# Kernel tuning notes

Measured on AMD Instinct MI355X. Metric: run time of the kernel, lower is better.

## Reference

```python
import jax, jax.numpy as jnp
import numpy as np

EPS_BN = 1e-5
EPS_COS = 1e-8
M_BINS = 10


def _bn(x, g, b):
    # eval-mode BatchNorm2d with running_mean=0, running_var=1
    s = g / jnp.sqrt(1.0 + EPS_BN)
    return x * s[None, :, None, None] + b[None, :, None, None]


def _dw(x, w, pad, dil):
    # depthwise conv, x [B,C,H,W], w [C,1,kh,kw]
    return jax.lax.conv_general_dilated(
        x, w, window_strides=(1, 1), padding=pad, rhs_dilation=dil,
        dimension_numbers=('NCHW', 'OIHW', 'NCHW'),
        feature_group_count=x.shape[1])


def setup_inputs() -> dict:
    key = jax.random.key(0)
    ks = jax.random.split(key, 20)
    B, INP, OUP, H, W = 16, 64, 64, 128, 128
    f32 = jnp.float32
    d = {}
    d['x'] = jax.random.normal(ks[0], (B, INP, H, W), f32)
    d['w_conv1'] = jax.random.normal(ks[1], (OUP, INP), f32) * 0.05
    d['pr_w1'] = jax.random.normal(ks[2], (OUP, 1, 1, 5), f32) * 0.2
    d['pr_w2'] = jax.random.normal(ks[3], (OUP, 1, 5, 1), f32) * 0.2
    d['pr_w3'] = jax.random.normal(ks[4], (OUP, 1, 1, 5), f32) * 0.2
    d['pr_w4'] = jax.random.normal(ks[5], (OUP, 1, 5, 1), f32) * 0.2
    d['pr_gamma'] = 1.0 + 0.1 * jax.random.normal(ks[6], (5, OUP), f32)
    d['pr_beta'] = 0.1 * jax.random.normal(ks[7], (5, OUP), f32)
    d['bn1_g'] = 1.0 + 0.1 * jax.random.normal(ks[8], (OUP,), f32)
    d['bn1_b'] = 0.1 * jax.random.normal(ks[9], (OUP,), f32)
    d['bn2_g'] = 1.0 + 0.1 * jax.random.normal(ks[10], (OUP,), f32)
    d['bn2_b'] = 0.1 * jax.random.normal(ks[11], (OUP,), f32)
    d['fc1_w'] = jax.random.normal(ks[12], (OUP, 2), f32) * 0.5
    d['fc1_b'] = 0.1 * jax.random.normal(ks[13], (OUP,), f32)
    d['phi1_w'] = jax.random.normal(ks[14], (OUP, OUP), f32) * 0.1
    d['phi1_b'] = 0.01 * jax.random.normal(ks[15], (OUP,), f32)
    d['phi2_w'] = jax.random.normal(ks[16], (OUP, OUP), f32) * 0.1
    d['phi2_b'] = 0.01 * jax.random.normal(ks[17], (OUP,), f32)
    d['phi3_w'] = jax.random.normal(ks[18], (OUP, OUP), f32) * 0.1
    d['phi3_b'] = 0.01 * jax.random.normal(ks[19], (OUP,), f32)
    d['w_conv2'] = jax.random.normal(jax.random.fold_in(key, 99), (OUP, 1), f32) * 0.1
    return d


def reference(x, w_conv1, pr_w1, pr_w2, pr_w3, pr_w4, pr_gamma, pr_beta,
              bn1_g, bn1_b, bn2_g, bn2_b, fc1_w, fc1_b,
              phi1_w, phi1_b, phi2_w, phi2_b, phi3_w, phi3_b, w_conv2):
    B, C, H, W = x.shape
    M = M_BINS
    OUP = w_conv1.shape[0]
    # conv1 (1x1) + Position_reinforcement branch
    x_c = jnp.einsum('oc,bchw->bohw', w_conv1, x)
    h = _bn(x_c, pr_gamma[0], pr_beta[0])
    h = _dw(h, pr_w1, ((0, 0), (2, 2)), (1, 1))
    h = _bn(h, pr_gamma[1], pr_beta[1])
    h = _dw(h, pr_w2, ((2, 2), (0, 0)), (1, 1))
    h = _bn(h, pr_gamma[2], pr_beta[2])
    h = _dw(h, pr_w3, ((0, 0), (4, 4)), (2, 2))
    h = _bn(h, pr_gamma[3], pr_beta[3])
    h = _dw(h, pr_w4, ((4, 4), (0, 0)), (2, 2))
    x_center = _bn(h, pr_gamma[4], pr_beta[4])
    # cosine similarity of each pixel feature with the global-avg feature
    g = jnp.mean(x, axis=(2, 3), keepdims=True)             # [B,C,1,1]
    num = jnp.sum(g * x, axis=1)                            # [B,H,W]
    gn = jnp.maximum(jnp.sqrt(jnp.sum(g * g, axis=1)), EPS_COS)
    xn = jnp.maximum(jnp.sqrt(jnp.sum(x * x, axis=1)), EPS_COS)
    S = num / (gn * xn)                                     # [B,H,W]
    Sf = S.reshape(B, H * W)
    # torch casts min/max with float() -> detached constants
    mn = jax.lax.stop_gradient(jnp.min(Sf, axis=1))
    mx = jax.lax.stop_gradient(jnp.max(Sf, axis=1))
    t = jnp.arange(M, dtype=x.dtype) / (M - 1)
    levels = mn[:, None] + (mx - mn)[:, None] * t[None, :]  # [B,M]
    diff = jnp.abs(levels[:, None, :] - Sf[:, :, None])     # [B,HW,M] soft bins
    V = jnp.where(diff < 0.5 / M, 1.0 - diff, jnp.zeros((), x.dtype))
    colsum = jnp.sum(V, axis=1)                             # [B,M]
    # torch normalizes by V.sum() while only columns 0..j are filled -> cumsum
    denom = jnp.cumsum(colsum, axis=1)
    Ch = jnp.stack([colsum / denom, levels], axis=-1)       # [B,M,2]
    Cf = Ch.reshape(-1, 2) @ fc1_w.T + fc1_b                # [B*M,OUP]
    Cq = Cf.reshape(B, OUP, M)                              # raw view as in torch
    p1 = jnp.einsum('oc,bcm->bom', phi1_w, Cq) + phi1_b[None, :, None]
    p2 = jnp.einsum('oc,bcm->bom', phi2_w, Cq) + phi2_b[None, :, None]
    X = jax.nn.softmax(jnp.einsum('bcm,bcn->bmn', p1, p2), axis=-1)  # [B,M,M]
    p3 = jnp.einsum('oc,bcm->bom', phi3_w, Cq) + phi3_b[None, :, None]
    Lp = jnp.einsum('bcm,bmn->bcn', p3, X)                  # [B,OUP,M]
    Vr = V.reshape(B, M, H * W)                             # raw view as in torch
    R = jnp.einsum('bcm,bmk->bck', Lp, Vr).reshape(B, OUP, H, W)
    x_tex = _bn(R, bn1_g, bn1_b)
    x_full = _bn(w_conv2[:, 0][None, :, None, None] * S[:, None, :, :], bn2_g, bn2_b)
    att = jax.nn.sigmoid(x_full + x_tex + x_center)
    return x * att
```

## Files before the change

### kernel.cpp

```cpp
#include <hip/hip_runtime.h>
#include <hip/hip_bf16.h>
#include <math.h>

#define NB   16
#define NC   64
#define NH   128
#define NW   128
#define NHW  16384
#define NM   10

__global__ __launch_bounds__(256) void k_gmean(const float* __restrict__ x,
                                               double* __restrict__ g) {
    int bc = blockIdx.x;
    const float* xp = x + (size_t)bc * NHW;
    double s = 0.0;
    for (int i = threadIdx.x; i < NHW / 4; i += 256) {
        float4 v = ((const float4*)xp)[i];
        s += (double)v.x + (double)v.y + (double)v.z + (double)v.w;
    }
    for (int off = 32; off; off >>= 1) s += __shfl_down(s, off);
    __shared__ double red[4];
    int wid = threadIdx.x >> 6, lane = threadIdx.x & 63;
    if (lane == 0) red[wid] = s;
    __syncthreads();
    if (threadIdx.x == 0)
        g[bc] = (red[0] + red[1] + red[2] + red[3]) * (1.0 / (double)NHW);
}

__global__ __launch_bounds__(256) void k_misc(const float* __restrict__ W,
                                              const double* __restrict__ g,
                                              float* __restrict__ Wt,
                                              double* __restrict__ gn) {
    if (blockIdx.x == 0) {
        for (int e = threadIdx.x; e < 64 * 64; e += 256) {
            int c = e >> 6, o = e & 63;
            Wt[c * 64 + o] = W[o * 64 + c];
        }
    } else if (threadIdx.x == 0) {
        int b = blockIdx.x - 1;
        const double* gb = g + b * NC;
        double gsq = 0.0;
        for (int c = 0; c < NC; ++c) gsq += gb[c] * gb[c];
        gn[b] = fmax(sqrt(gsq), 1e-8);
    }
}

__global__ __launch_bounds__(256) void k_conv1_S(
        const float* __restrict__ x, const float* __restrict__ Wt,
        const double* __restrict__ g, const double* __restrict__ gn,
        float* __restrict__ xc, double* __restrict__ S) {
    __shared__ __align__(16) float Xs[64 * 128];
    int bid = blockIdx.x;
    int b = bid >> 7, k0 = (bid & 127) * 128;
    int tid = threadIdx.x;
    const float* xb = x + (size_t)b * NC * NHW + k0;

    for (int e = tid; e < 64 * 32; e += 256) {
        int c = e >> 5, p4 = (e & 31) << 2;
        *(float4*)&Xs[c * 128 + p4] =
            *(const float4*)&xb[(size_t)c * NHW + p4];
    }
    __syncthreads();

    if (tid < 128) {
        const double* gb = g + b * NC;
        double num = 0.0, sq = 0.0;
#pragma unroll
        for (int c = 0; c < NC; ++c) {
            double v = (double)Xs[c * 128 + tid];
            num += gb[c] * v;
            sq  += v * v;
        }
        double xn = fmax(sqrt(sq), 1e-8);
        S[(size_t)b * NHW + k0 + tid] = num / (gn[b] * xn);
    }

    int o0 = __builtin_amdgcn_readfirstlane((tid >> 6) * 8);
    int px0 = (tid & 63) * 2;
    float acc[16][2];
#pragma unroll
    for (int i = 0; i < 16; ++i) { acc[i][0] = 0.f; acc[i][1] = 0.f; }

#pragma unroll 4
    for (int c = 0; c < NC; ++c) {
        float2 xa = *(float2*)&Xs[c * 128 + px0];
        const float* wr = Wt + c * 64 + o0;
        float wv[16];
#pragma unroll
        for (int i = 0; i < 8; ++i) wv[i] = wr[i];
#pragma unroll
        for (int i = 0; i < 8; ++i) wv[8 + i] = wr[32 + i];
#pragma unroll
        for (int i = 0; i < 16; ++i) {
            acc[i][0] = fmaf(wv[i], xa.x, acc[i][0]);
            acc[i][1] = fmaf(wv[i], xa.y, acc[i][1]);
        }
    }

    float* xcb = xc + (size_t)b * NC * NHW + k0;
#pragma unroll
    for (int i = 0; i < 16; ++i) {
        int o = o0 + ((i < 8) ? i : (24 + i));
        float2 s0; s0.x = acc[i][0]; s0.y = acc[i][1];
        *(float2*)&xcb[(size_t)o * NHW + px0] = s0;
    }
}

__global__ __launch_bounds__(256) void k_chain(
        const double* __restrict__ S,
        const float* __restrict__ fc1w, const float* __restrict__ fc1b,
        const float* __restrict__ ph1w, const float* __restrict__ ph1b,
        const float* __restrict__ ph2w, const float* __restrict__ ph2b,
        const float* __restrict__ ph3w, const float* __restrict__ ph3b,
        double* __restrict__ levelsOut, float* __restrict__ LpOut) {
    int b = blockIdx.x, tid = threadIdx.x;
    const double* Sb = S + b * NHW;

    double mn = 1e300, mx = -1e300;
    for (int i = tid; i < NHW; i += 256) {
        double v = Sb[i];
        mn = fmin(mn, v); mx = fmax(mx, v);
    }
    for (int off = 32; off; off >>= 1) {
        mn = fmin(mn, __shfl_down(mn, off));
        mx = fmax(mx, __shfl_down(mx, off));
    }
    __shared__ double rmn[4], rmx[4];
    int wid = tid >> 6, lane = tid & 63;
    if (lane == 0) { rmn[wid] = mn; rmx[wid] = mx; }
    __syncthreads();
    __shared__ double levS[NM];
    if (tid == 0) {
        double a = fmin(fmin(rmn[0], rmn[1]), fmin(rmn[2], rmn[3]));
        double z = fmax(fmax(rmx[0], rmx[1]), fmax(rmx[2], rmx[3]));
        for (int m = 0; m < NM; ++m) levS[m] = a + (z - a) * ((double)m / 9.0);
    }
    __syncthreads();
    double lv[NM];
#pragma unroll
    for (int m = 0; m < NM; ++m) lv[m] = levS[m];

    double bins[NM];
#pragma unroll
    for (int m = 0; m < NM; ++m) bins[m] = 0.0;
    for (int i = tid; i < NHW; i += 256) {
        double v = Sb[i];
#pragma unroll
        for (int m = 0; m < NM; ++m) {
            double d = fabs(lv[m] - v);
            if (d < 0.05) bins[m] += 1.0 - d;
        }
    }
#pragma unroll
    for (int m = 0; m < NM; ++m)
        for (int off = 32; off; off >>= 1) bins[m] += __shfl_down(bins[m], off);
    __shared__ double wb[4][NM];
    if (lane == 0) {
#pragma unroll
        for (int m = 0; m < NM; ++m) wb[wid][m] = bins[m];
    }
    __syncthreads();
    __shared__ float ratio[NM];
    if (tid == 0) {
        double den = 0.0;
        for (int m = 0; m < NM; ++m) {
            double cs = wb[0][m] + wb[1][m] + wb[2][m] + wb[3][m];
            den += cs;
            ratio[m] = (float)(cs / den);
        }
    }
    __syncthreads();

    __shared__ float CfL[640];
    for (int idx = tid; idx < 640; idx += 256) {
        int rm = idx >> 6, o = idx & 63;
        CfL[idx] = ratio[rm] * fc1w[o*2+0] + (float)levS[rm] * fc1w[o*2+1] + fc1b[o];
    }
    __syncthreads();

    __shared__ float P1[640], P2[640], P3[640];
    for (int idx = tid; idx < 640; idx += 256) {
        int o = idx / 10, m = idx - o * 10;
        float a1 = ph1b[o], a2 = ph2b[o], a3 = ph3b[o];
        for (int c2 = 0; c2 < NC; ++c2) {
            float cq = CfL[c2*10 + m];
            a1 = fmaf(ph1w[o*NC + c2], cq, a1);
            a2 = fmaf(ph2w[o*NC + c2], cq, a2);
            a3 = fmaf(ph3w[o*NC + c2], cq, a3);
        }
        P1[idx] = a1; P2[idx] = a2; P3[idx] = a3;
    }
    __syncthreads();

    __shared__ float XL[100];
    if (tid < 100) {
        int m = tid / 10, n = tid - (tid/10)*10;
        float acc = 0.f;
        for (int c2 = 0; c2 < NC; ++c2)
            acc = fmaf(P1[c2*10 + m], P2[c2*10 + n], acc);
        XL[tid] = acc;
    }
    __syncthreads();
    if (tid < NM) {
        float mxr = XL[tid*10];
        for (int n = 1; n < NM; ++n) mxr = fmaxf(mxr, XL[tid*10 + n]);
        float e[NM], sum = 0.f;
        for (int n = 0; n < NM; ++n) { e[n] = expf(XL[tid*10+n] - mxr); sum += e[n]; }
        for (int n = 0; n < NM; ++n) XL[tid*10+n] = e[n] / sum;
    }
    __syncthreads();

    for (int idx = tid; idx < 640; idx += 256) {
        int c2 = idx / 10, n = idx - (idx/10)*10;
        float acc = 0.f;
#pragma unroll
        for (int m = 0; m < NM; ++m) acc = fmaf(P3[c2*10 + m], XL[m*10 + n], acc);
        LpOut[b*640 + idx] = acc;
    }
    if (tid < NM) levelsOut[b*NM + tid] = levS[tid];
}

__global__ __launch_bounds__(256) void k_vgath(
        const double* __restrict__ S, const double* __restrict__ levels,
        float* __restrict__ vg, float* __restrict__ Sf) {
    int P = blockIdx.x * 256 + threadIdx.x;
    int b = P >> 14, k = P & (NHW - 1);
    __shared__ double levL[NM];
    if (threadIdx.x < NM) levL[threadIdx.x] = levels[b*NM + threadIdx.x];
    __syncthreads();
    const double* Sb = S + (size_t)b * NHW;
    float* vgb = vg + (size_t)b * NM * NHW;
#pragma unroll
    for (int i = 0; i < NM; ++i) {
        int j = i * NHW + k;
        int p = j / 10;
        int m = j - p * 10;
        double d = fabs(levL[m] - Sb[p]);
        vgb[i * NHW + k] = (d < 0.05) ? (float)(1.0 - d) : 0.f;
    }
    Sf[P] = (float)Sb[k];
}

__global__ __launch_bounds__(256) void k_dwfinal(
        const float* __restrict__ xc, const float* __restrict__ x,
        const float* __restrict__ vg, const float* __restrict__ Sf,
        const float* __restrict__ Lp,
        const float* __restrict__ pw1, const float* __restrict__ pw2,
        const float* __restrict__ pw3, const float* __restrict__ pw4,
        const float* __restrict__ gamma, const float* __restrict__ beta,
        const float* __restrict__ bn1g, const float* __restrict__ bn1b,
        const float* __restrict__ bn2g, const float* __restrict__ bn2b,
        const float* __restrict__ wconv2, float* __restrict__ out) {
    int tile = blockIdx.x, c = blockIdx.y, b = blockIdx.z;
    int R0 = (tile >> 1) * 32, C0 = (tile & 1) * 64;
    const float inv = 0.9999950000374997f;
    float s0 = gamma[0*NC+c]*inv, b0 = beta[0*NC+c];
    float s1 = gamma[1*NC+c]*inv, b1 = beta[1*NC+c];
    float s2 = gamma[2*NC+c]*inv, b2 = beta[2*NC+c];
    float s3 = gamma[3*NC+c]*inv, b3 = beta[3*NC+c];
    float s4 = gamma[4*NC+c]*inv, b4 = beta[4*NC+c];
    float w1[5], w2[5], w3[5], w4[5];
#pragma unroll
    for (int q = 0; q < 5; ++q) {
        w1[q] = pw1[c*5+q]; w2[q] = pw2[c*5+q];
        w3[q] = pw3[c*5+q]; w4[q] = pw4[c*5+q];
    }
    float Ac = wconv2[c] * (bn2g[c] * inv);
    float Bc = bn2b[c] + bn1b[c];
    float S1 = bn1g[c] * inv;

    __shared__ __align__(16) float A[44*76];
    __shared__ __align__(16) float Bf[44*72];
    __shared__ float LpL[NM];
    const float* src = xc + ((size_t)(b*NC + c)) * NHW;
    int tid = threadIdx.x;

    if (tid < NM) LpL[tid] = Lp[b*640 + c*10 + tid];

    for (int t = tid; t < 44*19; t += 256) {
        int r = t / 19, g2 = t - r*19;
        int gy = R0 - 6 + r, gx0 = C0 - 6 + 4*g2;
        float4 v = make_float4(0.f, 0.f, 0.f, 0.f);
        bool rowOK = (unsigned)gy < NH;
        if (rowOK) {
            const float* rowp = src + gy*NW;
            if ((unsigned)gx0 <= (unsigned)(NW-4)) {
                v = *(const float4*)(rowp + gx0);
            } else {
                float* pv = (float*)&v;
#pragma unroll
                for (int u = 0; u < 4; ++u) {
                    int gx = gx0 + u;
                    if ((unsigned)gx < NW) pv[u] = rowp[gx];
                }
            }
        }
        float4 w;
        w.x = (rowOK && (unsigned)(gx0+0) < NW) ? fmaf(v.x, s0, b0) : 0.f;
        w.y = (rowOK && (unsigned)(gx0+1) < NW) ? fmaf(v.y, s0, b0) : 0.f;
        w.z = (rowOK && (unsigned)(gx0+2) < NW) ? fmaf(v.z, s0, b0) : 0.f;
        w.w = (rowOK && (unsigned)(gx0+3) < NW) ? fmaf(v.w, s0, b0) : 0.f;
        *(float4*)&A[r*76 + 4*g2] = w;
    }
    __syncthreads();

    for (int t = tid; t < 44*9; t += 256) {
        int r = t / 9, gp = t - r*9;
        float xw[12];
        *(float4*)&xw[0] = *(float4*)&A[r*76 + 8*gp];
        *(float4*)&xw[4] = *(float4*)&A[r*76 + 8*gp + 4];
        *(float4*)&xw[8] = *(float4*)&A[r*76 + 8*gp + 8];
        int gy = R0 - 6 + r;
        bool rowOK = (unsigned)gy < NH;
        float o[8];
#pragma unroll
        for (int u = 0; u < 8; ++u) {
            float acc = 0.f;
#pragma unroll
            for (int q = 0; q < 5; ++q) acc = fmaf(w1[q], xw[u+q], acc);
            int gx = C0 - 4 + 8*gp + u;
            o[u] = (rowOK && (unsigned)gx < NW) ? fmaf(acc, s1, b1) : 0.f;
        }
        *(float4*)&Bf[r*72 + 8*gp]     = *(float4*)&o[0];
        *(float4*)&Bf[r*72 + 8*gp + 4] = *(float4*)&o[4];
    }
    __syncthreads();

    if (tid < 180) {
        int rg = tid / 18, g2 = tid - rg*18;
        float ys[8][4];
#pragma unroll
        for (int m = 0; m < 8; ++m)
            *(float4*)&ys[m][0] = *(float4*)&Bf[(4*rg + m)*72 + 4*g2];
        bool colOK[4];
#pragma unroll
        for (int u = 0; u < 4; ++u)
            colOK[u] = (unsigned)(C0 - 4 + 4*g2 + u) < NW;
#pragma unroll
        for (int rr = 0; rr < 4; ++rr) {
            int gy = R0 - 4 + 4*rg + rr;
            bool rowOK = (unsigned)gy < NH;
            float o[4];
#pragma unroll
            for (int u = 0; u < 4; ++u) {
                float acc = 0.f;
#pragma unroll
                for (int p = 0; p < 5; ++p) acc = fmaf(w2[p], ys[rr+p][u], acc);
                o[u] = (rowOK && colOK[u]) ? fmaf(acc, s2, b2) : 0.f;
            }
            *(float4*)&A[(4*rg + rr)*72 + 4*g2] = *(float4*)o;
        }
    }
    __syncthreads();

    for (int t = tid; t < 40*8; t += 256) {
        int r = t >> 3, gp = t & 7;
        float xw[16];
        *(float4*)&xw[0]  = *(float4*)&A[r*72 + 8*gp];
        *(float4*)&xw[4]  = *(float4*)&A[r*72 + 8*gp + 4];
        *(float4*)&xw[8]  = *(float4*)&A[r*72 + 8*gp + 8];
        *(float4*)&xw[12] = *(float4*)&A[r*72 + 8*gp + 12];
        int gy = R0 - 4 + r;
        bool rowOK = (unsigned)gy < NH;
        float o[8];
#pragma unroll
        for (int u = 0; u < 8; ++u) {
            float acc = 0.f;
#pragma unroll
            for (int q = 0; q < 5; ++q) acc = fmaf(w3[q], xw[u+2*q], acc);
            o[u] = rowOK ? fmaf(acc, s3, b3) : 0.f;
        }
        *(float4*)&Bf[r*64 + 8*gp]     = *(float4*)&o[0];
        *(float4*)&Bf[r*64 + 8*gp + 4] = *(float4*)&o[4];
    }
    __syncthreads();

    {
        int gr = tid >> 4, g2 = tid & 15;
        int base = (gr & 1) + 4*(gr >> 1);
        float ys[6][4];
#pragma unroll
        for (int m = 0; m < 6; ++m)
            *(float4*)&ys[m][0] = *(float4*)&Bf[(base + 2*m)*64 + 4*g2];
        const float* vgb = vg + (size_t)b * NM * NHW;
        const float* Sfb = Sf + (size_t)b * NHW;
#pragma unroll
        for (int j = 0; j < 2; ++j) {
            int ro = base + 2*j;
            int kbase = (R0 + ro) * NW + C0 + 4*g2;
            size_t xbase = (size_t)(b*NC + c) * NHW + kbase;
            float4 xv = *(const float4*)&x[xbase];
            float4 skv = *(const float4*)&Sfb[kbase];
            const float* xvp = (const float*)&xv;
            const float* skp = (const float*)&skv;
            float vr[NM][4];
#pragma unroll
            for (int i = 0; i < NM; ++i)
                *(float4*)&vr[i][0] = *(const float4*)&vgb[i * NHW + kbase];
            float res[4];
#pragma unroll
            for (int u = 0; u < 4; ++u) {
                float acc = 0.f;
#pragma unroll
                for (int p = 0; p < 5; ++p) acc = fmaf(w4[p], ys[j+p][u], acc);
                float xcen = fmaf(acc, s4, b4);
                float R = 0.f;
#pragma unroll
                for (int i = 0; i < NM; ++i) R = fmaf(LpL[i], vr[i][u], R);
                float pre = fmaf(Ac, skp[u], Bc) + S1 * R + xcen;
                float att = 1.0f / (1.0f + expf(-pre));
                res[u] = xvp[u] * att;
            }
            *(float4*)&out[xbase] = *(float4*)res;
        }
    }
}

extern "C" void kernel_launch(void* const* d_in, const int* in_sizes, int n_in,
                              void* d_out, int out_size, void* d_ws, size_t ws_size,
                              hipStream_t stream) {
    (void)in_sizes; (void)n_in; (void)out_size; (void)ws_size;
    const float* x      = (const float*)d_in[0];
    const float* wconv1 = (const float*)d_in[1];
    const float* pw1    = (const float*)d_in[2];
    const float* pw2    = (const float*)d_in[3];
    const float* pw3    = (const float*)d_in[4];
    const float* pw4    = (const float*)d_in[5];
    const float* pgam   = (const float*)d_in[6];
    const float* pbet   = (const float*)d_in[7];
    const float* bn1g   = (const float*)d_in[8];
    const float* bn1b   = (const float*)d_in[9];
    const float* bn2g   = (const float*)d_in[10];
    const float* bn2b   = (const float*)d_in[11];
    const float* fc1w   = (const float*)d_in[12];
    const float* fc1b   = (const float*)d_in[13];
    const float* ph1w   = (const float*)d_in[14];
    const float* ph1b   = (const float*)d_in[15];
    const float* ph2w   = (const float*)d_in[16];
    const float* ph2b   = (const float*)d_in[17];
    const float* ph3w   = (const float*)d_in[18];
    const float* ph3b   = (const float*)d_in[19];
    const float* wconv2 = (const float*)d_in[20];
    float* out = (float*)d_out;

    float*  ws  = (float*)d_ws;
    float*  xc  = ws;
    double* Sd  = (double*)(ws + 16777216);
    double* g   = Sd + NB * NHW;
    double* lev = g + NB * NC;
    double* gn  = lev + NB * NM;
    float*  Lp  = (float*)(gn + NB);
    float*  vg  = Lp + NB * 640;
    float*  Sf  = vg + NB * NM * NHW;
    float*  Wt  = Sf + NB * NHW;

    k_gmean<<<NB * NC, 256, 0, stream>>>(x, g);
    k_misc<<<17, 256, 0, stream>>>(wconv1, g, Wt, gn);
    k_conv1_S<<<NB * NHW / 128, 256, 0, stream>>>(x, Wt, g, gn, xc, Sd);
    k_chain<<<NB, 256, 0, stream>>>(Sd, fc1w, fc1b, ph1w, ph1b, ph2w, ph2b,
                                    ph3w, ph3b, lev, Lp);
    k_vgath<<<NB * NHW / 256, 256, 0, stream>>>(Sd, lev, vg, Sf);
    k_dwfinal<<<dim3(8, NC, NB), 256, 0, stream>>>(
        xc, x, vg, Sf, Lp, pw1, pw2, pw3, pw4, pgam, pbet,
        bn1g, bn1b, bn2g, bn2b, wconv2, out);
}
```

Baseline: 172.9 us.

## Retile conv1, split min/max and histogram across blocks, pair channels in dwfinal

The 1x1 conv kernel now handles 256 pixels per block with an 8x8 register tile, and it transposes the weights into shared memory itself, so the separate transpose work is dropped. The per-batch min/max and soft-histogram reductions move out of the 16-block chain kernel into two 64-block kernels that write partial results. The chain kernel then only combines those partials. The depthwise/final kernel now processes two channels per block on 32x32 tiles, sharing the vg and Sf loads between the two channels. Each of these adds parallelism or reuse, at the cost of an extra launch and changed reduction order.

After: 183.5 us. 6.1% more time.

```diff
diff --git a/kernel.cpp b/kernel.cpp
--- a/kernel.cpp
+++ b/kernel.cpp
@@ -8,6 +8,7 @@
 #define NW   128
 #define NHW  16384
 #define NM   10
+#define SA   52
 
 __global__ __launch_bounds__(256) void k_gmean(const float* __restrict__ x,
                                                double* __restrict__ g) {
@@ -27,17 +28,10 @@
         g[bc] = (red[0] + red[1] + red[2] + red[3]) * (1.0 / (double)NHW);
 }
 
-__global__ __launch_bounds__(256) void k_misc(const float* __restrict__ W,
-                                              const double* __restrict__ g,
-                                              float* __restrict__ Wt,
-                                              double* __restrict__ gn) {
-    if (blockIdx.x == 0) {
-        for (int e = threadIdx.x; e < 64 * 64; e += 256) {
-            int c = e >> 6, o = e & 63;
-            Wt[c * 64 + o] = W[o * 64 + c];
-        }
-    } else if (threadIdx.x == 0) {
-        int b = blockIdx.x - 1;
+__global__ __launch_bounds__(64) void k_misc(const double* __restrict__ g,
+                                             double* __restrict__ gn) {
+    if (threadIdx.x == 0) {
+        int b = blockIdx.x;
         const double* gb = g + b * NC;
         double gsq = 0.0;
         for (int c = 0; c < NC; ++c) gsq += gb[c] * gb[c];
@@ -46,125 +40,163 @@
 }
 
 __global__ __launch_bounds__(256) void k_conv1_S(
-        const float* __restrict__ x, const float* __restrict__ Wt,
+        const float* __restrict__ x, const float* __restrict__ W,
         const double* __restrict__ g, const double* __restrict__ gn,
         float* __restrict__ xc, double* __restrict__ S) {
-    __shared__ __align__(16) float Xs[64 * 128];
+    __shared__ __align__(16) float Xs[32 * 256];
+    __shared__ __align__(16) float WtL[64 * 64];
     int bid = blockIdx.x;
-    int b = bid >> 7, k0 = (bid & 127) * 128;
+    int b = bid >> 6, k0 = (bid & 63) * 256;
     int tid = threadIdx.x;
     const float* xb = x + (size_t)b * NC * NHW + k0;
 
-    for (int e = tid; e < 64 * 32; e += 256) {
-        int c = e >> 5, p4 = (e & 31) << 2;
-        *(float4*)&Xs[c * 128 + p4] =
-            *(const float4*)&xb[(size_t)c * NHW + p4];
-    }
-    __syncthreads();
-
-    if (tid < 128) {
-        const double* gb = g + b * NC;
-        double num = 0.0, sq = 0.0;
-#pragma unroll
-        for (int c = 0; c < NC; ++c) {
-            double v = (double)Xs[c * 128 + tid];
-            num += gb[c] * v;
+    for (int e = tid; e < 4096; e += 256) {
+        int c = e >> 6, o = e & 63;
+        WtL[e] = W[o * 64 + c];
+    }
+
+    int pg = tid & 31, og = tid >> 5;
+    int px0 = pg * 8, o0 = og * 8;
+    float acc[8][8];
+#pragma unroll
+    for (int i = 0; i < 8; ++i)
+#pragma unroll
+        for (int j = 0; j < 8; ++j) acc[i][j] = 0.f;
+    double num = 0.0, sq = 0.0;
+    const double* gb = g + b * NC;
+
+#pragma unroll
+    for (int h = 0; h < 2; ++h) {
+        if (h) __syncthreads();
+        for (int e = tid; e < 2048; e += 256) {
+            int cl = e >> 6, p4 = (e & 63) << 2;
+            *(float4*)&Xs[cl * 256 + p4] =
+                *(const float4*)&xb[(size_t)(32*h + cl) * NHW + p4];
+        }
+        __syncthreads();
+
+#pragma unroll 8
+        for (int cl = 0; cl < 32; ++cl) {
+            double v = (double)Xs[cl * 256 + tid];
+            num += gb[32*h + cl] * v;
             sq  += v * v;
         }
-        double xn = fmax(sqrt(sq), 1e-8);
-        S[(size_t)b * NHW + k0 + tid] = num / (gn[b] * xn);
-    }
-
-    int o0 = __builtin_amdgcn_readfirstlane((tid >> 6) * 8);
-    int px0 = (tid & 63) * 2;
-    float acc[16][2];
-#pragma unroll
-    for (int i = 0; i < 16; ++i) { acc[i][0] = 0.f; acc[i][1] = 0.f; }
-
 #pragma unroll 4
-    for (int c = 0; c < NC; ++c) {
-        float2 xa = *(float2*)&Xs[c * 128 + px0];
-        const float* wr = Wt + c * 64 + o0;
-        float wv[16];
-#pragma unroll
-        for (int i = 0; i < 8; ++i) wv[i] = wr[i];
-#pragma unroll
-        for (int i = 0; i < 8; ++i) wv[8 + i] = wr[32 + i];
-#pragma unroll
-        for (int i = 0; i < 16; ++i) {
-            acc[i][0] = fmaf(wv[i], xa.x, acc[i][0]);
-            acc[i][1] = fmaf(wv[i], xa.y, acc[i][1]);
-        }
-    }
+        for (int cl = 0; cl < 32; ++cl) {
+            int cg = 32*h + cl;
+            float4 xa  = *(float4*)&Xs[cl * 256 + px0];
+            float4 xb2 = *(float4*)&Xs[cl * 256 + px0 + 4];
+            float4 wa  = *(float4*)&WtL[cg * 64 + o0];
+            float4 wb2 = *(float4*)&WtL[cg * 64 + o0 + 4];
+            float xr[8] = {xa.x, xa.y, xa.z, xa.w, xb2.x, xb2.y, xb2.z, xb2.w};
+            float wr[8] = {wa.x, wa.y, wa.z, wa.w, wb2.x, wb2.y, wb2.z, wb2.w};
+#pragma unroll
+            for (int i = 0; i < 8; ++i)
+#pragma unroll
+                for (int j = 0; j < 8; ++j)
+                    acc[i][j] = fmaf(wr[i], xr[j], acc[i][j]);
+        }
+    }
+
+    double xn = fmax(sqrt(sq), 1e-8);
+    S[(size_t)b * NHW + k0 + tid] = num / (gn[b] * xn);
 
     float* xcb = xc + (size_t)b * NC * NHW + k0;
 #pragma unroll
-    for (int i = 0; i < 16; ++i) {
-        int o = o0 + ((i < 8) ? i : (24 + i));
-        float2 s0; s0.x = acc[i][0]; s0.y = acc[i][1];
-        *(float2*)&xcb[(size_t)o * NHW + px0] = s0;
+    for (int i = 0; i < 8; ++i) {
+        float4 s0, s1;
+        s0.x = acc[i][0]; s0.y = acc[i][1]; s0.z = acc[i][2]; s0.w = acc[i][3];
+        s1.x = acc[i][4]; s1.y = acc[i][5]; s1.z = acc[i][6]; s1.w = acc[i][7];
+        *(float4*)&xcb[(size_t)(o0 + i) * NHW + px0] = s0;
+        *(float4*)&xcb[(size_t)(o0 + i) * NHW + px0 + 4] = s1;
+    }
+}
+
+__global__ __launch_bounds__(256) void k_minmax(const double* __restrict__ S,
+                                                double* __restrict__ pmn,
+                                                double* __restrict__ pmx) {
+    int blk = blockIdx.x, b = blk >> 2, part = blk & 3;
+    const double* Sb = S + (size_t)b * NHW + part * 4096;
+    int tid = threadIdx.x;
+    double mn = 1e300, mx = -1e300;
+    for (int i = tid; i < 4096; i += 256) {
+        double v = Sb[i];
+        mn = fmin(mn, v); mx = fmax(mx, v);
+    }
+    for (int off = 32; off; off >>= 1) {
+        mn = fmin(mn, __shfl_down(mn, off));
+        mx = fmax(mx, __shfl_down(mx, off));
+    }
+    __shared__ double rmn[4], rmx[4];
+    int wid = tid >> 6, lane = tid & 63;
+    if (lane == 0) { rmn[wid] = mn; rmx[wid] = mx; }
+    __syncthreads();
+    if (tid == 0) {
+        pmn[blk] = fmin(fmin(rmn[0], rmn[1]), fmin(rmn[2], rmn[3]));
+        pmx[blk] = fmax(fmax(rmx[0], rmx[1]), fmax(rmx[2], rmx[3]));
+    }
+}
+
+__global__ __launch_bounds__(256) void k_hist(const double* __restrict__ S,
+                                              const double* __restrict__ pmn,
+                                              const double* __restrict__ pmx,
+                                              double* __restrict__ pbins) {
+    int blk = blockIdx.x, b = blk >> 2, part = blk & 3;
+    double a = fmin(fmin(pmn[4*b], pmn[4*b+1]), fmin(pmn[4*b+2], pmn[4*b+3]));
+    double z = fmax(fmax(pmx[4*b], pmx[4*b+1]), fmax(pmx[4*b+2], pmx[4*b+3]));
+    double lv[NM];
+#pragma unroll
+    for (int m = 0; m < NM; ++m) lv[m] = a + (z - a) * ((double)m / 9.0);
+
+    const double* Sb = S + (size_t)b * NHW + part * 4096;
+    int tid = threadIdx.x;
+    double bins[NM];
+#pragma unroll
+    for (int m = 0; m < NM; ++m) bins[m] = 0.0;
+    for (int i = tid; i < 4096; i += 256) {
+        double v = Sb[i];
+#pragma unroll
+        for (int m = 0; m < NM; ++m) {
+            double d = fabs(lv[m] - v);
+            if (d < 0.05) bins[m] += 1.0 - d;
+        }
+    }
+#pragma unroll
+    for (int m = 0; m < NM; ++m)
+        for (int off = 32; off; off >>= 1) bins[m] += __shfl_down(bins[m], off);
+    __shared__ double wb[4][NM];
+    int wid = tid >> 6, lane = tid & 63;
+    if (lane == 0) {
+#pragma unroll
+        for (int m = 0; m < NM; ++m) wb[wid][m] = bins[m];
+    }
+    __syncthreads();
+    if (tid == 0) {
+#pragma unroll
+        for (int m = 0; m < NM; ++m)
+            pbins[blk * NM + m] = wb[0][m] + wb[1][m] + wb[2][m] + wb[3][m];
     }
 }
 
 __global__ __launch_bounds__(256) void k_chain(
-        const double* __restrict__ S,
+        const double* __restrict__ pmn, const double* __restrict__ pmx,
+        const double* __restrict__ pbins,
         const float* __restrict__ fc1w, const float* __restrict__ fc1b,
         const float* __restrict__ ph1w, const float* __restrict__ ph1b,
         const float* __restrict__ ph2w, const float* __restrict__ ph2b,
         const float* __restrict__ ph3w, const float* __restrict__ ph3b,
         double* __restrict__ levelsOut, float* __restrict__ LpOut) {
     int b = blockIdx.x, tid = threadIdx.x;
-    const double* Sb = S + b * NHW;
-
-    double mn = 1e300, mx = -1e300;
-    for (int i = tid; i < NHW; i += 256) {
-        double v = Sb[i];
-        mn = fmin(mn, v); mx = fmax(mx, v);
-    }
-    for (int off = 32; off; off >>= 1) {
-        mn = fmin(mn, __shfl_down(mn, off));
-        mx = fmax(mx, __shfl_down(mx, off));
-    }
-    __shared__ double rmn[4], rmx[4];
-    int wid = tid >> 6, lane = tid & 63;
-    if (lane == 0) { rmn[wid] = mn; rmx[wid] = mx; }
-    __syncthreads();
     __shared__ double levS[NM];
-    if (tid == 0) {
-        double a = fmin(fmin(rmn[0], rmn[1]), fmin(rmn[2], rmn[3]));
-        double z = fmax(fmax(rmx[0], rmx[1]), fmax(rmx[2], rmx[3]));
-        for (int m = 0; m < NM; ++m) levS[m] = a + (z - a) * ((double)m / 9.0);
-    }
-    __syncthreads();
-    double lv[NM];
-#pragma unroll
-    for (int m = 0; m < NM; ++m) lv[m] = levS[m];
-
-    double bins[NM];
-#pragma unroll
-    for (int m = 0; m < NM; ++m) bins[m] = 0.0;
-    for (int i = tid; i < NHW; i += 256) {
-        double v = Sb[i];
-#pragma unroll
-        for (int m = 0; m < NM; ++m) {
-            double d = fabs(lv[m] - v);
-            if (d < 0.05) bins[m] += 1.0 - d;
-        }
-    }
-#pragma unroll
-    for (int m = 0; m < NM; ++m)
-        for (int off = 32; off; off >>= 1) bins[m] += __shfl_down(bins[m], off);
-    __shared__ double wb[4][NM];
-    if (lane == 0) {
-#pragma unroll
-        for (int m = 0; m < NM; ++m) wb[wid][m] = bins[m];
-    }
-    __syncthreads();
     __shared__ float ratio[NM];
     if (tid == 0) {
+        double a = fmin(fmin(pmn[4*b], pmn[4*b+1]), fmin(pmn[4*b+2], pmn[4*b+3]));
+        double z = fmax(fmax(pmx[4*b], pmx[4*b+1]), fmax(pmx[4*b+2], pmx[4*b+3]));
+        for (int m = 0; m < NM; ++m) levS[m] = a + (z - a) * ((double)m / 9.0);
         double den = 0.0;
         for (int m = 0; m < NM; ++m) {
-            double cs = wb[0][m] + wb[1][m] + wb[2][m] + wb[3][m];
+            double cs = ((pbins[(4*b)*NM+m] + pbins[(4*b+1)*NM+m])
+                        + pbins[(4*b+2)*NM+m]) + pbins[(4*b+3)*NM+m];
             den += cs;
             ratio[m] = (float)(cs / den);
         }
@@ -251,167 +283,198 @@
         const float* __restrict__ bn1g, const float* __restrict__ bn1b,
         const float* __restrict__ bn2g, const float* __restrict__ bn2b,
         const float* __restrict__ wconv2, float* __restrict__ out) {
-    int tile = blockIdx.x, c = blockIdx.y, b = blockIdx.z;
-    int R0 = (tile >> 1) * 32, C0 = (tile & 1) * 64;
+    int tile = blockIdx.x, cp = blockIdx.y, b = blockIdx.z;
+    int R0 = (tile >> 2) * 32, C0 = (tile & 3) * 32;
     const float inv = 0.9999950000374997f;
-    float s0 = gamma[0*NC+c]*inv, b0 = beta[0*NC+c];
-    float s1 = gamma[1*NC+c]*inv, b1 = beta[1*NC+c];
-    float s2 = gamma[2*NC+c]*inv, b2 = beta[2*NC+c];
-    float s3 = gamma[3*NC+c]*inv, b3 = beta[3*NC+c];
-    float s4 = gamma[4*NC+c]*inv, b4 = beta[4*NC+c];
-    float w1[5], w2[5], w3[5], w4[5];
-#pragma unroll
-    for (int q = 0; q < 5; ++q) {
-        w1[q] = pw1[c*5+q]; w2[q] = pw2[c*5+q];
-        w3[q] = pw3[c*5+q]; w4[q] = pw4[c*5+q];
-    }
-    float Ac = wconv2[c] * (bn2g[c] * inv);
-    float Bc = bn2b[c] + bn1b[c];
-    float S1 = bn1g[c] * inv;
-
-    __shared__ __align__(16) float A[44*76];
-    __shared__ __align__(16) float Bf[44*72];
-    __shared__ float LpL[NM];
-    const float* src = xc + ((size_t)(b*NC + c)) * NHW;
+    float s0[2], v0[2], s1[2], v1[2], s2[2], v2[2], s3[2], v3[2], s4[2], v4[2];
+    float w1[2][5], w2[2][5], w3[2][5], w4[2][5];
+    float Acc[2], Bcc[2], S1c[2];
+#pragma unroll
+    for (int ch = 0; ch < 2; ++ch) {
+        int c = cp*2 + ch;
+        s0[ch] = gamma[0*NC+c]*inv; v0[ch] = beta[0*NC+c];
+        s1[ch] = gamma[1*NC+c]*inv; v1[ch] = beta[1*NC+c];
+        s2[ch] = gamma[2*NC+c]*inv; v2[ch] = beta[2*NC+c];
+        s3[ch] = gamma[3*NC+c]*inv; v3[ch] = beta[3*NC+c];
+        s4[ch] = gamma[4*NC+c]*inv; v4[ch] = beta[4*NC+c];
+#pragma unroll
+        for (int q = 0; q < 5; ++q) {
+            w1[ch][q] = pw1[c*5+q]; w2[ch][q] = pw2[c*5+q];
+            w3[ch][q] = pw3[c*5+q]; w4[ch][q] = pw4[c*5+q];
+        }
+        Acc[ch] = wconv2[c] * (bn2g[c] * inv);
+        Bcc[ch] = bn2b[c] + bn1b[c];
+        S1c[ch] = bn1g[c] * inv;
+    }
+
+    __shared__ __align__(16) float A[2*44*SA];
+    __shared__ __align__(16) float Bfs[2*44*SA];
+    __shared__ float LpL[2][NM];
     int tid = threadIdx.x;
-
-    if (tid < NM) LpL[tid] = Lp[b*640 + c*10 + tid];
-
-    for (int t = tid; t < 44*19; t += 256) {
-        int r = t / 19, g2 = t - r*19;
-        int gy = R0 - 6 + r, gx0 = C0 - 6 + 4*g2;
-        float4 v = make_float4(0.f, 0.f, 0.f, 0.f);
+    if (tid < 2*NM) LpL[tid/NM][tid%NM] = Lp[b*640 + (cp*2 + tid/NM)*10 + tid%NM];
+    const float* src0 = xc + (size_t)(b*NC + cp*2) * NHW;
+    const float* src1 = src0 + NHW;
+
+    for (int t = tid; t < 484; t += 256) {
+        int r = t / 11, g4 = t - r*11;
+        int gy = R0 - 6 + r, gx0 = C0 - 6 + 4*g4;
         bool rowOK = (unsigned)gy < NH;
-        if (rowOK) {
-            const float* rowp = src + gy*NW;
-            if ((unsigned)gx0 <= (unsigned)(NW-4)) {
-                v = *(const float4*)(rowp + gx0);
-            } else {
-                float* pv = (float*)&v;
-#pragma unroll
-                for (int u = 0; u < 4; ++u) {
-                    int gx = gx0 + u;
-                    if ((unsigned)gx < NW) pv[u] = rowp[gx];
+        bool full4 = (unsigned)gx0 <= (unsigned)(NW-4);
+        bool m0 = (unsigned)(gx0+0) < NW, m1 = (unsigned)(gx0+1) < NW;
+        bool m2 = (unsigned)(gx0+2) < NW, m3 = (unsigned)(gx0+3) < NW;
+        const float* srcs[2] = {src0, src1};
+#pragma unroll
+        for (int ch = 0; ch < 2; ++ch) {
+            float4 v = make_float4(0.f, 0.f, 0.f, 0.f);
+            if (rowOK) {
+                const float* rowp = srcs[ch] + gy*NW;
+                if (full4) v = *(const float4*)(rowp + gx0);
+                else {
+                    float* pv = (float*)&v;
+#pragma unroll
+                    for (int u = 0; u < 4; ++u) {
+                        int gx = gx0 + u;
+                        if ((unsigned)gx < NW) pv[u] = rowp[gx];
+                    }
                 }
             }
-        }
-        float4 w;
-        w.x = (rowOK && (unsigned)(gx0+0) < NW) ? fmaf(v.x, s0, b0) : 0.f;
-        w.y = (rowOK && (unsigned)(gx0+1) < NW) ? fmaf(v.y, s0, b0) : 0.f;
-        w.z = (rowOK && (unsigned)(gx0+2) < NW) ? fmaf(v.z, s0, b0) : 0.f;
-        w.w = (rowOK && (unsigned)(gx0+3) < NW) ? fmaf(v.w, s0, b0) : 0.f;
-        *(float4*)&A[r*76 + 4*g2] = w;
-    }
-    __syncthreads();
-
-    for (int t = tid; t < 44*9; t += 256) {
-        int r = t / 9, gp = t - r*9;
-        float xw[12];
-        *(float4*)&xw[0] = *(float4*)&A[r*76 + 8*gp];
-        *(float4*)&xw[4] = *(float4*)&A[r*76 + 8*gp + 4];
-        *(float4*)&xw[8] = *(float4*)&A[r*76 + 8*gp + 8];
+            float4 w;
+            w.x = (rowOK && m0) ? fmaf(v.x, s0[ch], v0[ch]) : 0.f;
+            w.y = (rowOK && m1) ? fmaf(v.y, s0[ch], v0[ch]) : 0.f;
+            w.z = (rowOK && m2) ? fmaf(v.z, s0[ch], v0[ch]) : 0.f;
+            w.w = (rowOK && m3) ? fmaf(v.w, s0[ch], v0[ch]) : 0.f;
+            *(float4*)&A[ch*44*SA + r*SA + 4*g4] = w;
+        }
+    }
+    __syncthreads();
+
+    for (int t = tid; t < 220; t += 256) {
+        int r = t / 5, gp = t - r*5;
         int gy = R0 - 6 + r;
         bool rowOK = (unsigned)gy < NH;
-        float o[8];
-#pragma unroll
-        for (int u = 0; u < 8; ++u) {
-            float acc = 0.f;
-#pragma unroll
-            for (int q = 0; q < 5; ++q) acc = fmaf(w1[q], xw[u+q], acc);
-            int gx = C0 - 4 + 8*gp + u;
-            o[u] = (rowOK && (unsigned)gx < NW) ? fmaf(acc, s1, b1) : 0.f;
-        }
-        *(float4*)&Bf[r*72 + 8*gp]     = *(float4*)&o[0];
-        *(float4*)&Bf[r*72 + 8*gp + 4] = *(float4*)&o[4];
-    }
-    __syncthreads();
-
-    if (tid < 180) {
-        int rg = tid / 18, g2 = tid - rg*18;
-        float ys[8][4];
-#pragma unroll
-        for (int m = 0; m < 8; ++m)
-            *(float4*)&ys[m][0] = *(float4*)&Bf[(4*rg + m)*72 + 4*g2];
+        bool cm[8];
+#pragma unroll
+        for (int u = 0; u < 8; ++u)
+            cm[u] = rowOK && ((unsigned)(C0 - 4 + 8*gp + u) < NW);
+#pragma unroll
+        for (int ch = 0; ch < 2; ++ch) {
+            float xw[12];
+            *(float4*)&xw[0] = *(float4*)&A[ch*44*SA + r*SA + 8*gp];
+            *(float4*)&xw[4] = *(float4*)&A[ch*44*SA + r*SA + 8*gp + 4];
+            *(float4*)&xw[8] = *(float4*)&A[ch*44*SA + r*SA + 8*gp + 8];
+            float o[8];
+#pragma unroll
+            for (int u = 0; u < 8; ++u) {
+                float acc = 0.f;
+#pragma unroll
+                for (int q = 0; q < 5; ++q) acc = fmaf(w1[ch][q], xw[u+q], acc);
+                o[u] = cm[u] ? fmaf(acc, s1[ch], v1[ch]) : 0.f;
+            }
+            *(float4*)&Bfs[ch*44*SA + r*SA + 8*gp]     = *(float4*)&o[0];
+            *(float4*)&Bfs[ch*44*SA + r*SA + 8*gp + 4] = *(float4*)&o[4];
+        }
+    }
+    __syncthreads();
+
+    if (tid < 100) {
+        int rg = tid / 10, g2 = tid - rg*10;
         bool colOK[4];
 #pragma unroll
         for (int u = 0; u < 4; ++u)
             colOK[u] = (unsigned)(C0 - 4 + 4*g2 + u) < NW;
 #pragma unroll
-        for (int rr = 0; rr < 4; ++rr) {
-            int gy = R0 - 4 + 4*rg + rr;
-            bool rowOK = (unsigned)gy < NH;
-            float o[4];
-#pragma unroll
-            for (int u = 0; u < 4; ++u) {
-                float acc = 0.f;
-#pragma unroll
-                for (int p = 0; p < 5; ++p) acc = fmaf(w2[p], ys[rr+p][u], acc);
-                o[u] = (rowOK && colOK[u]) ? fmaf(acc, s2, b2) : 0.f;
+        for (int ch = 0; ch < 2; ++ch) {
+            float ys[8][4];
+#pragma unroll
+            for (int m = 0; m < 8; ++m)
+                *(float4*)&ys[m][0] = *(float4*)&Bfs[ch*44*SA + (4*rg + m)*SA + 4*g2];
+#pragma unroll
+            for (int rr = 0; rr < 4; ++rr) {
+                int gy = R0 - 4 + 4*rg + rr;
+                bool rowOK = (unsigned)gy < NH;
+                float o[4];
+#pragma unroll
+                for (int u = 0; u < 4; ++u) {
+                    float acc = 0.f;
+#pragma unroll
+                    for (int p = 0; p < 5; ++p) acc = fmaf(w2[ch][p], ys[rr+p][u], acc);
+                    o[u] = (rowOK && colOK[u]) ? fmaf(acc, s2[ch], v2[ch]) : 0.f;
+                }
+                *(float4*)&A[ch*44*SA + (4*rg + rr)*SA + 4*g2] = *(float4*)o;
             }
-            *(float4*)&A[(4*rg + rr)*72 + 4*g2] = *(float4*)o;
-        }
-    }
-    __syncthreads();
-
-    for (int t = tid; t < 40*8; t += 256) {
-        int r = t >> 3, gp = t & 7;
-        float xw[16];
-        *(float4*)&xw[0]  = *(float4*)&A[r*72 + 8*gp];
-        *(float4*)&xw[4]  = *(float4*)&A[r*72 + 8*gp + 4];
-        *(float4*)&xw[8]  = *(float4*)&A[r*72 + 8*gp + 8];
-        *(float4*)&xw[12] = *(float4*)&A[r*72 + 8*gp + 12];
+        }
+    }
+    __syncthreads();
+
+    if (tid < 160) {
+        int r = tid >> 2, gp = tid & 3;
         int gy = R0 - 4 + r;
         bool rowOK = (unsigned)gy < NH;
-        float o[8];
-#pragma unroll
-        for (int u = 0; u < 8; ++u) {
-            float acc = 0.f;
-#pragma unroll
-            for (int q = 0; q < 5; ++q) acc = fmaf(w3[q], xw[u+2*q], acc);
-            o[u] = rowOK ? fmaf(acc, s3, b3) : 0.f;
-        }
-        *(float4*)&Bf[r*64 + 8*gp]     = *(float4*)&o[0];
-        *(float4*)&Bf[r*64 + 8*gp + 4] = *(float4*)&o[4];
-    }
-    __syncthreads();
-
-    {
-        int gr = tid >> 4, g2 = tid & 15;
+#pragma unroll
+        for (int ch = 0; ch < 2; ++ch) {
+            float xw[16];
+            *(float4*)&xw[0]  = *(float4*)&A[ch*44*SA + r*SA + 8*gp];
+            *(float4*)&xw[4]  = *(float4*)&A[ch*44*SA + r*SA + 8*gp + 4];
+            *(float4*)&xw[8]  = *(float4*)&A[ch*44*SA + r*SA + 8*gp + 8];
+            *(float4*)&xw[12] = *(float4*)&A[ch*44*SA + r*SA + 8*gp + 12];
+            float o[8];
+#pragma unroll
+            for (int u = 0; u < 8; ++u) {
+                float acc = 0.f;
+#pragma unroll
+                for (int q = 0; q < 5; ++q) acc = fmaf(w3[ch][q], xw[u+2*q], acc);
+                o[u] = rowOK ? fmaf(acc, s3[ch], v3[ch]) : 0.f;
+            }
+            *(float4*)&Bfs[ch*44*SA + r*SA + 8*gp]     = *(float4*)&o[0];
+            *(float4*)&Bfs[ch*44*SA + r*SA + 8*gp + 4] = *(float4*)&o[4];
+        }
+    }
+    __syncthreads();
+
+    if (tid < 128) {
+        int gr = tid >> 3, g2 = tid & 7;
         int base = (gr & 1) + 4*(gr >> 1);
-        float ys[6][4];
-#pragma unroll
-        for (int m = 0; m < 6; ++m)
-            *(float4*)&ys[m][0] = *(float4*)&Bf[(base + 2*m)*64 + 4*g2];
+        float ys[2][6][4];
+#pragma unroll
+        for (int ch = 0; ch < 2; ++ch)
+#pragma unroll
+            for (int m = 0; m < 6; ++m)
+                *(float4*)&ys[ch][m][0] =
+                    *(float4*)&Bfs[ch*44*SA + (base + 2*m)*SA + 4*g2];
         const float* vgb = vg + (size_t)b * NM * NHW;
         const float* Sfb = Sf + (size_t)b * NHW;
 #pragma unroll
         for (int j = 0; j < 2; ++j) {
             int ro = base + 2*j;
             int kbase = (R0 + ro) * NW + C0 + 4*g2;
-            size_t xbase = (size_t)(b*NC + c) * NHW + kbase;
-            float4 xv = *(const float4*)&x[xbase];
-            float4 skv = *(const float4*)&Sfb[kbase];
-            const float* xvp = (const float*)&xv;
-            const float* skp = (const float*)&skv;
             float vr[NM][4];
 #pragma unroll
             for (int i = 0; i < NM; ++i)
                 *(float4*)&vr[i][0] = *(const float4*)&vgb[i * NHW + kbase];
-            float res[4];
-#pragma unroll
-            for (int u = 0; u < 4; ++u) {
-                float acc = 0.f;
-#pragma unroll
-                for (int p = 0; p < 5; ++p) acc = fmaf(w4[p], ys[j+p][u], acc);
-                float xcen = fmaf(acc, s4, b4);
-                float R = 0.f;
-#pragma unroll
-                for (int i = 0; i < NM; ++i) R = fmaf(LpL[i], vr[i][u], R);
-                float pre = fmaf(Ac, skp[u], Bc) + S1 * R + xcen;
-                float att = 1.0f / (1.0f + expf(-pre));
-                res[u] = xvp[u] * att;
+            float4 skv = *(const float4*)&Sfb[kbase];
+            const float* skp = (const float*)&skv;
+#pragma unroll
+            for (int ch = 0; ch < 2; ++ch) {
+                size_t xbase = (size_t)(b*NC + cp*2 + ch) * NHW + kbase;
+                float4 xv = *(const float4*)&x[xbase];
+                const float* xvp = (const float*)&xv;
+                float res[4];
+#pragma unroll
+                for (int u = 0; u < 4; ++u) {
+                    float acc = 0.f;
+#pragma unroll
+                    for (int p = 0; p < 5; ++p)
+                        acc = fmaf(w4[ch][p], ys[ch][j+p][u], acc);
+                    float xcen = fmaf(acc, s4[ch], v4[ch]);
+                    float R = 0.f;
+#pragma unroll
+                    for (int i = 0; i < NM; ++i) R = fmaf(LpL[ch][i], vr[i][u], R);
+                    float pre = fmaf(Acc[ch], skp[u], Bcc[ch]) + S1c[ch] * R + xcen;
+                    float att = 1.0f / (1.0f + expf(-pre));
+                    res[u] = xvp[u] * att;
+                }
+                *(float4*)&out[xbase] = *(float4*)res;
             }
-            *(float4*)&out[xbase] = *(float4*)res;
         }
     }
 }
@@ -443,24 +506,29 @@
     const float* wconv2 = (const float*)d_in[20];
     float* out = (float*)d_out;
 
-    float*  ws  = (float*)d_ws;
-    float*  xc  = ws;
-    double* Sd  = (double*)(ws + 16777216);
-    double* g   = Sd + NB * NHW;
-    double* lev = g + NB * NC;
-    double* gn  = lev + NB * NM;
-    float*  Lp  = (float*)(gn + NB);
-    float*  vg  = Lp + NB * 640;
-    float*  Sf  = vg + NB * NM * NHW;
-    float*  Wt  = Sf + NB * NHW;
+    float*  ws    = (float*)d_ws;
+    float*  xc    = ws;
+    double* Sd    = (double*)(ws + 16777216);
+    double* g     = Sd + NB * NHW;
+    double* lev   = g + NB * NC;
+    double* gn    = lev + NB * NM;
+    double* pmn   = gn + NB;
+    double* pmx   = pmn + 64;
+    double* pbins = pmx + 64;
+    float*  Lp    = (float*)(pbins + 640);
+    float*  vg    = Lp + NB * 640;
+    float*  Sf    = vg + NB * NM * NHW;
 
     k_gmean<<<NB * NC, 256, 0, stream>>>(x, g);
-    k_misc<<<17, 256, 0, stream>>>(wconv1, g, Wt, gn);
-    k_conv1_S<<<NB * NHW / 128, 256, 0, stream>>>(x, Wt, g, gn, xc, Sd);
-    k_chain<<<NB, 256, 0, stream>>>(Sd, fc1w, fc1b, ph1w, ph1b, ph2w, ph2b,
-                                    ph3w, ph3b, lev, Lp);
+    k_misc<<<NB, 64, 0, stream>>>(g, gn);
+    k_conv1_S<<<NB * NHW / 256, 256, 0, stream>>>(x, wconv1, g, gn, xc, Sd);
+    k_minmax<<<NB * 4, 256, 0, stream>>>(Sd, pmn, pmx);
+    k_hist<<<NB * 4, 256, 0, stream>>>(Sd, pmn, pmx, pbins);
+    k_chain<<<NB, 256, 0, stream>>>(pmn, pmx, pbins, fc1w, fc1b,
+                                    ph1w, ph1b, ph2w, ph2b, ph3w, ph3b,
+                                    lev, Lp);
     k_vgath<<<NB * NHW / 256, 256, 0, stream>>>(Sd, lev, vg, Sf);
-    k_dwfinal<<<dim3(8, NC, NB), 256, 0, stream>>>(
+    k_dwfinal<<<dim3(16, 32, NB), 256, 0, stream>>>(
         xc, x, vg, Sf, Lp, pw1, pw2, pw3, pw4, pgam, pbet,
         bn1g, bn1b, bn2g, bn2b, wconv2, out);
 }
```
